# Performance work log

Measured on AMD Instinct MI355X. Metric: run time of the kernel, lower is better.

The kernel has to match this reference:

```python
import jax, jax.numpy as jnp
import numpy as np

N_IN = 512
N_OUT = 256
T = 2048
B = 32


def setup_inputs() -> dict:
    key = jax.random.key(0)
    ks = jax.random.split(key, 9)
    s_in = 1.0 / np.sqrt(N_IN)
    inp = {
        "xt": jax.random.normal(ks[0], (T, B, N_IN), dtype=jnp.float32),
        "ct_forward": jax.random.normal(ks[1], (1, B, N_OUT), dtype=jnp.float32),
        # weights stored torch-style as [out, in]
        "Wx": jax.random.uniform(ks[2], (N_OUT, N_IN), jnp.float32, -s_in, s_in),
        "Wf": jax.random.uniform(ks[3], (N_OUT, N_IN), jnp.float32, -s_in, s_in),
        "bf": jax.random.uniform(ks[4], (N_OUT,), jnp.float32, -s_in, s_in),
        "Wr": jax.random.uniform(ks[5], (N_OUT, N_IN), jnp.float32, -s_in, s_in),
        "br": jax.random.uniform(ks[6], (N_OUT,), jnp.float32, -s_in, s_in),
        "Wc": jax.random.uniform(ks[7], (N_OUT, N_IN), jnp.float32, -s_in, s_in),
        "bc": jax.random.uniform(ks[8], (N_OUT,), jnp.float32, -s_in, s_in),
    }
    return inp


def reference(xt, ct_forward, Wx, Wf, bf, Wr, br, Wc, bc):
    # Batched projections over all timesteps (the GEMM part of SRU).
    x_proj = jnp.einsum("tbi,oi->tbo", xt, Wx)              # [T,B,n_out]
    f = jax.nn.sigmoid(jnp.einsum("tbi,oi->tbo", xt, Wf) + bf)
    r = jax.nn.sigmoid(jnp.einsum("tbi,oi->tbo", xt, Wr) + br)
    cx = jnp.einsum("tbi,oi->tbo", xt, Wc) + bc

    def step(c, inp):
        x_t, ft, rt, cxt = inp
        c = ft * c + (1.0 - ft) * x_t
        h = rt * jnp.tanh(c) + (1.0 - rt) * cxt
        return c, h

    c_final, ht = jax.lax.scan(step, ct_forward[0], (x_proj, f, r, cx))
    # dropout=0.0 -> identity; forward returns (ht, ct)
    return ht, c_final
```

## Files before the change

### kernel.cpp

```cpp
#include <hip/hip_runtime.h>
#include <stdint.h>

#define T_STEPS 2048
#define BATCH   32
#define NIN     512
#define NOUT    256
#define MROWS   (T_STEPS*BATCH)
#define BO      (BATCH*NOUT)
#define NCHUNK  32
#define CHLEN   (T_STEPS/NCHUNK)

typedef _Float16 f16x8 __attribute__((ext_vector_type(8)));
typedef _Float16 f16x4 __attribute__((ext_vector_type(4)));
typedef float    fx4   __attribute__((ext_vector_type(4)));

#define LDSP(p) ((__attribute__((address_space(3))) void*)(p))
#define GLBP(p) ((const __attribute__((address_space(1))) void*)(p))

#define BAR()        asm volatile("s_barrier" ::: "memory")
#define WAITLGKM0()  do { asm volatile("s_waitcnt lgkmcnt(0)" ::: "memory"); __builtin_amdgcn_sched_barrier(0); } while(0)
#define WAITVM(n)    do { asm volatile("s_waitcnt vmcnt(" #n ")" ::: "memory"); __builtin_amdgcn_sched_barrier(0); } while(0)

__global__ __launch_bounds__(256) void convert_w(
    const float* __restrict__ Wx, const float* __restrict__ Wf,
    const float* __restrict__ Wr, const float* __restrict__ Wc,
    _Float16* __restrict__ Wcat)
{
    int idx = blockIdx.x * 256 + threadIdx.x;
    int n  = idx >> 7;
    int k4 = (idx & 127) * 4;
    int g = n >> 8, o = n & 255;
    const float* W = (g == 0) ? Wx : (g == 1) ? Wf : (g == 2) ? Wr : Wc;
    float4 v = *(const float4*)(W + o * NIN + k4);
    f16x4 h;
    h[0] = (_Float16)v.x; h[1] = (_Float16)v.y;
    h[2] = (_Float16)v.z; h[3] = (_Float16)v.w;
    *(f16x4*)(Wcat + n * NIN + k4) = h;
}

#define BM 256
#define BN 256
#define BK 64
#define NGT 32

__global__ __launch_bounds__(512, 1) void gemm_proj(
    const float*    __restrict__ xt,
    const _Float16* __restrict__ Wcat,
    const float* __restrict__ bfv, const float* __restrict__ brv, const float* __restrict__ bcv,
    _Float16* __restrict__ xp_h, _Float16* __restrict__ f_h,
    _Float16* __restrict__ r_h,  _Float16* __restrict__ cx_h)
{
    __shared__ char lds[131072];

    const int tid  = threadIdx.x;
    const int lane = tid & 63;
    const int w    = tid >> 6;
    const int wrq  = w >> 2;
    const int wcq  = w & 3;
    const int lr = lane & 15, lk = lane >> 4;

    int wg = (blockIdx.x & 7) * 32 + (blockIdx.x >> 3);
    const int  cg   = wg & 3;
    const int  mgrp = wg >> 2;
    const long m0 = (long)mgrp * 1024;
    const int  n0 = cg * BN;

    const char* baseAg = (const char*)xt + (m0 + (tid >> 4)) * 2048 + (tid & 15) * 16;
    const int awbase = (tid >> 4) * 128 + (((tid & 15) * 8) ^ (((tid >> 4) & 7) << 4));

    const int rl8  = lane >> 3;
    const int scol = (((lane & 7) ^ rl8) << 4);
    const char* baseB = (const char*)Wcat + ((long)(n0 + w * 8 + rl8)) * 1024 + scol;

    float4 av0[4], av1[4];
#define ALOAD_H(gi, half, dst) do {                                          \
        const char* _b = baseAg + (long)((gi) >> 3) * 524288                 \
                         + ((gi) & 7) * 256 + (half) * 262144;               \
        _Pragma("unroll")                                                    \
        for (int jj = 0; jj < 4; ++jj)                                       \
            dst[jj] = *(const float4*)(_b + jj * 65536);                     \
    } while (0)
#define AWRITE_H(gi, half, src) do {                                         \
        char* _d = lds + ((gi) & 1) * 32768 + (half) * 16384 + awbase;       \
        _Pragma("unroll")                                                    \
        for (int jj = 0; jj < 4; ++jj) {                                     \
            f16x4 _h;                                                        \
            _h[0] = (_Float16)src[jj].x; _h[1] = (_Float16)src[jj].y;        \
            _h[2] = (_Float16)src[jj].z; _h[3] = (_Float16)src[jj].w;        \
            *(f16x4*)(_d + jj * 4096) = _h;                                  \
        }                                                                    \
    } while (0)
#define STAGE_B(g, h) do {                                                   \
        char* _d = lds + 65536 + ((g) & 1) * 32768 + (h) * 16384 + w * 1024; \
        const char* _s = baseB + ((g) & 7) * 128 + (long)(h) * 131072;       \
        __builtin_amdgcn_global_load_lds(GLBP(_s),         LDSP(_d),        16, 0, 0); \
        __builtin_amdgcn_global_load_lds(GLBP(_s + 65536), LDSP(_d + 8192), 16, 0, 0); \
    } while (0)

    fx4 acc[2][2][4][2];
    #pragma unroll
    for (int a = 0; a < 2; ++a)
        #pragma unroll
        for (int b = 0; b < 2; ++b)
            #pragma unroll
            for (int c = 0; c < 4; ++c)
                #pragma unroll
                for (int d = 0; d < 2; ++d)
                    acc[a][b][c][d] = (fx4){0.f, 0.f, 0.f, 0.f};

    f16x8 Ar[4][2];
    f16x8 B0r[2][2];
    f16x8 B1r[2][2];

#define READ_A(c2, h) do {                                                   \
        _Pragma("unroll")                                                    \
        for (int mf = 0; mf < 4; ++mf) {                                     \
            int rl = wrq * 64 + mf * 16 + lr;                                \
            int rb = (c2) * 32768 + (h) * 16384 + rl * 128;                  \
            _Pragma("unroll")                                                \
            for (int kk = 0; kk < 2; ++kk)                                   \
                Ar[mf][kk] = *(const f16x8*)(lds + rb +                      \
                    ((kk * 64 + lk * 16) ^ ((rl & 7) << 4)));                \
        }                                                                    \
    } while (0)
#define READ_B(c2, h, dst) do {                                              \
        _Pragma("unroll")                                                    \
        for (int nf = 0; nf < 2; ++nf) {                                     \
            int rl = wcq * 32 + nf * 16 + lr;                                \
            int rb = 65536 + (c2) * 32768 + (h) * 16384 + rl * 128;          \
            _Pragma("unroll")                                                \
            for (int kk = 0; kk < 2; ++kk)                                   \
                dst[nf][kk] = *(const f16x8*)(lds + rb +                     \
                    ((kk * 64 + lk * 16) ^ ((rl & 7) << 4)));                \
        }                                                                    \
    } while (0)
#define MMACC(Qr, Qc, Br) do {                                               \
        __builtin_amdgcn_s_setprio(1);                                       \
        _Pragma("unroll")                                                    \
        for (int kk = 0; kk < 2; ++kk)                                       \
            _Pragma("unroll")                                                \
            for (int mf = 0; mf < 4; ++mf)                                   \
                _Pragma("unroll")                                            \
                for (int nf = 0; nf < 2; ++nf)                               \
                    acc[Qr][Qc][mf][nf] = __builtin_amdgcn_mfma_f32_16x16x32_f16( \
                        Br[nf][kk], Ar[mf][kk], acc[Qr][Qc][mf][nf], 0, 0, 0);    \
        __builtin_amdgcn_s_setprio(0);                                       \
    } while (0)

    const int g_out = cg;
    _Float16* outp = (g_out == 0) ? xp_h : (g_out == 1) ? f_h : (g_out == 2) ? r_h : cx_h;
    const float* bias = (g_out == 1) ? bfv : (g_out == 2) ? brv : (g_out == 3) ? bcv : nullptr;

    ALOAD_H(0, 0, av0); ALOAD_H(0, 1, av1);
    STAGE_B(0, 0); STAGE_B(0, 1);
    WAITVM(4);
    AWRITE_H(0, 0, av0); AWRITE_H(0, 1, av1);
    STAGE_B(1, 0);
    WAITVM(2);
    WAITLGKM0();
    BAR();

    for (int g = 0; g < NGT; ++g) {
        const int c2 = g & 1;
        READ_A(c2, 0);
        READ_B(c2, 0, B0r);
        if (g + 1 < NGT) { ALOAD_H(g + 1, 0, av0); STAGE_B(g + 1, 1); }
        WAITLGKM0();
        MMACC(0, 0, B0r);
        READ_B(c2, 1, B1r);
        if (g + 1 < NGT) ALOAD_H(g + 1, 1, av1);
        WAITLGKM0();
        MMACC(0, 1, B1r);
        READ_A(c2, 1);
        BAR();
        WAITLGKM0();
        MMACC(1, 0, B0r);
        if (g + 2 < NGT) STAGE_B(g + 2, 0);
        MMACC(1, 1, B1r);
        if (g + 2 < NGT) { WAITVM(2); } else { WAITVM(0); }
        if (g + 1 < NGT) { AWRITE_H(g + 1, 0, av0); AWRITE_H(g + 1, 1, av1); }
        WAITLGKM0();
        BAR();
        if ((g & 7) == 7) {
            const long mbase = m0 + (long)(g >> 3) * 256;
            #pragma unroll
            for (int Qr = 0; Qr < 2; ++Qr) {
                #pragma unroll
                for (int Qc = 0; Qc < 2; ++Qc) {
                    #pragma unroll
                    for (int nf = 0; nf < 2; ++nf) {
                        const int ob = Qc * 128 + wcq * 32 + nf * 16 + lk * 4;
                        float4 bv4 = (g_out == 0) ? (float4){0.f, 0.f, 0.f, 0.f}
                                                  : *(const float4*)(bias + ob);
                        #pragma unroll
                        for (int mf = 0; mf < 4; ++mf) {
                            long row = mbase + Qr * 128 + wrq * 64 + mf * 16 + lr;
                            fx4 v = acc[Qr][Qc][mf][nf];
                            f16x4 hv;
                            if (g_out == 1 || g_out == 2) {
                                float p0 = v[0] + bv4.x, p1 = v[1] + bv4.y;
                                float p2 = v[2] + bv4.z, p3 = v[3] + bv4.w;
                                hv[0] = (_Float16)(__builtin_amdgcn_rcpf(1.0f + __expf(-p0)));
                                hv[1] = (_Float16)(__builtin_amdgcn_rcpf(1.0f + __expf(-p1)));
                                hv[2] = (_Float16)(__builtin_amdgcn_rcpf(1.0f + __expf(-p2)));
                                hv[3] = (_Float16)(__builtin_amdgcn_rcpf(1.0f + __expf(-p3)));
                            } else {
                                hv[0] = (_Float16)(v[0] + bv4.x);
                                hv[1] = (_Float16)(v[1] + bv4.y);
                                hv[2] = (_Float16)(v[2] + bv4.z);
                                hv[3] = (_Float16)(v[3] + bv4.w);
                            }
                            *(f16x4*)(outp + row * NOUT + ob) = hv;
                            acc[Qr][Qc][mf][nf] = (fx4){0.f, 0.f, 0.f, 0.f};
                        }
                    }
                }
            }
        }
    }
}

__global__ __launch_bounds__(256) void chunk_scan_a(
    const _Float16* __restrict__ f_h, const _Float16* __restrict__ xp_h,
    float* __restrict__ chunkA, float* __restrict__ chunkB)
{
    int tid2 = blockIdx.x * 256 + threadIdx.x;
    int ch = tid2 >> 11;
    int b4 = (tid2 & 2047) << 2;
    long base = (long)ch * CHLEN * BO + b4;
    fx4 a = (fx4){1.f, 1.f, 1.f, 1.f};
    fx4 cc = (fx4){0.f, 0.f, 0.f, 0.f};
    for (int s = 0; s < CHLEN; ++s) {
        long i = base + (long)s * BO;
        f16x4 fv = *(const f16x4*)(f_h + i);
        f16x4 xv = *(const f16x4*)(xp_h + i);
        #pragma unroll
        for (int q = 0; q < 4; ++q) {
            float f = (float)fv[q], x = (float)xv[q];
            cc[q] = f * cc[q] + (1.f - f) * x;
            a[q] *= f;
        }
    }
    *(fx4*)(chunkA + ch * BO + b4) = a;
    *(fx4*)(chunkB + ch * BO + b4) = cc;
}

__global__ __launch_bounds__(256) void chunk_prop(
    const float* __restrict__ ct0,
    const float* __restrict__ chunkA, const float* __restrict__ chunkB,
    float* __restrict__ cin, float* __restrict__ c_final)
{
    int bo = blockIdx.x * 256 + threadIdx.x;
    float c = ct0[bo];
    #pragma unroll
    for (int ch = 0; ch < NCHUNK; ++ch) {
        cin[ch * BO + bo] = c;
        c = chunkA[ch * BO + bo] * c + chunkB[ch * BO + bo];
    }
    c_final[bo] = c;
}

__global__ __launch_bounds__(256) void chunk_scan_h(
    const _Float16* __restrict__ xp_h, const _Float16* __restrict__ f_h,
    const _Float16* __restrict__ r_h,  const _Float16* __restrict__ cx_h,
    const float* __restrict__ cin, float* __restrict__ ht)
{
    int tid2 = blockIdx.x * 256 + threadIdx.x;
    int ch = tid2 >> 11;
    int b4 = (tid2 & 2047) << 2;
    long base = (long)ch * CHLEN * BO + b4;
    fx4 c = *(const fx4*)(cin + ch * BO + b4);
    for (int s = 0; s < CHLEN; ++s) {
        long i = base + (long)s * BO;
        f16x4 fv  = *(const f16x4*)(f_h + i);
        f16x4 xv  = *(const f16x4*)(xp_h + i);
        f16x4 rv  = *(const f16x4*)(r_h + i);
        f16x4 cxv = *(const f16x4*)(cx_h + i);
        fx4 h4;
        #pragma unroll
        for (int q = 0; q < 4; ++q) {
            float f = (float)fv[q], x = (float)xv[q];
            float r = (float)rv[q], cx = (float)cxv[q];
            c[q] = f * c[q] + (1.f - f) * x;
            float e = __expf(2.f * c[q]);
            float th = (e - 1.f) * __builtin_amdgcn_rcpf(e + 1.f);
            h4[q] = r * th + (1.f - r) * cx;
        }
        *(fx4*)(ht + i) = h4;
    }
}

extern "C" void kernel_launch(void* const* d_in, const int* in_sizes, int n_in,
                              void* d_out, int out_size, void* d_ws, size_t ws_size,
                              hipStream_t stream) {
    const float* xt  = (const float*)d_in[0];
    const float* ct0 = (const float*)d_in[1];
    const float* Wx  = (const float*)d_in[2];
    const float* Wf  = (const float*)d_in[3];
    const float* bf_ = (const float*)d_in[4];
    const float* Wr  = (const float*)d_in[5];
    const float* br_ = (const float*)d_in[6];
    const float* Wc  = (const float*)d_in[7];
    const float* bc_ = (const float*)d_in[8];

    float* ht      = (float*)d_out;
    float* c_final = ht + (size_t)MROWS * NOUT;

    char* ws = (char*)d_ws;
    _Float16* Wcat = (_Float16*)ws;
    _Float16* xp_h = (_Float16*)(ws + (1 << 20));
    _Float16* f_h  = xp_h + (size_t)MROWS * NOUT;
    _Float16* r_h  = f_h  + (size_t)MROWS * NOUT;
    _Float16* cx_h = r_h  + (size_t)MROWS * NOUT;
    float* chunkA  = (float*)(cx_h + (size_t)MROWS * NOUT);
    float* chunkB  = chunkA + NCHUNK * BO;
    float* cin     = chunkB + NCHUNK * BO;

    convert_w<<<512, 256, 0, stream>>>(Wx, Wf, Wr, Wc, Wcat);
    gemm_proj<<<256, 512, 0, stream>>>(
        xt, Wcat, bf_, br_, bc_, xp_h, f_h, r_h, cx_h);
    chunk_scan_a<<<256, 256, 0, stream>>>(f_h, xp_h, chunkA, chunkB);
    chunk_prop<<<BO / 256, 256, 0, stream>>>(ct0, chunkA, chunkB, cin, c_final);
    chunk_scan_h<<<256, 256, 0, stream>>>(xp_h, f_h, r_h, cx_h, cin, ht);
}
```

Measured before the change: 183.8 us.

## Prefetch A tiles two stages ahead with double-buffered register sets

The GEMM main loop now issues global loads of the fp32 A tile two iterations ahead instead of one, alternating between two register buffers (sa/sb) by unrolling the loop by two. The vmcnt waits are loosened so the in-flight A loads overlap with a full tile of MFMA work, hiding global load latency. The cost is doubled register use for staging A, which may lower occupancy or cause spills.

Measured after the change: 335.7 us. 82.6% more time.

```diff
diff --git a/kernel.cpp b/kernel.cpp
--- a/kernel.cpp
+++ b/kernel.cpp
@@ -72,7 +72,8 @@
     const int scol = (((lane & 7) ^ rl8) << 4);
     const char* baseB = (const char*)Wcat + ((long)(n0 + w * 8 + rl8)) * 1024 + scol;
 
-    float4 av0[4], av1[4];
+    float4 sa_h0[4], sa_h1[4];
+    float4 sb_h0[4], sb_h1[4];
 #define ALOAD_H(gi, half, dst) do {                                          \
         const char* _b = baseAg + (long)((gi) >> 3) * 524288                 \
                          + ((gi) & 7) * 256 + (half) * 262144;               \
@@ -151,72 +152,83 @@
     _Float16* outp = (g_out == 0) ? xp_h : (g_out == 1) ? f_h : (g_out == 2) ? r_h : cx_h;
     const float* bias = (g_out == 1) ? bfv : (g_out == 2) ? brv : (g_out == 3) ? bcv : nullptr;
 
-    ALOAD_H(0, 0, av0); ALOAD_H(0, 1, av1);
+#define EPILOGUE(g) do {                                                     \
+        const long mbase = m0 + (long)((g) >> 3) * 256;                      \
+        _Pragma("unroll")                                                    \
+        for (int Qr = 0; Qr < 2; ++Qr)                                       \
+            _Pragma("unroll")                                                \
+            for (int Qc = 0; Qc < 2; ++Qc)                                   \
+                _Pragma("unroll")                                            \
+                for (int nf = 0; nf < 2; ++nf) {                             \
+                    const int ob = Qc * 128 + wcq * 32 + nf * 16 + lk * 4;   \
+                    float4 bv4 = (g_out == 0) ? (float4){0.f, 0.f, 0.f, 0.f} \
+                                              : *(const float4*)(bias + ob); \
+                    _Pragma("unroll")                                        \
+                    for (int mf = 0; mf < 4; ++mf) {                         \
+                        long row = mbase + Qr * 128 + wrq * 64 + mf * 16 + lr; \
+                        fx4 v = acc[Qr][Qc][mf][nf];                         \
+                        f16x4 hv;                                            \
+                        if (g_out == 1 || g_out == 2) {                      \
+                            float p0 = v[0] + bv4.x, p1 = v[1] + bv4.y;      \
+                            float p2 = v[2] + bv4.z, p3 = v[3] + bv4.w;      \
+                            hv[0] = (_Float16)(__builtin_amdgcn_rcpf(1.0f + __expf(-p0))); \
+                            hv[1] = (_Float16)(__builtin_amdgcn_rcpf(1.0f + __expf(-p1))); \
+                            hv[2] = (_Float16)(__builtin_amdgcn_rcpf(1.0f + __expf(-p2))); \
+                            hv[3] = (_Float16)(__builtin_amdgcn_rcpf(1.0f + __expf(-p3))); \
+                        } else {                                             \
+                            hv[0] = (_Float16)(v[0] + bv4.x);                \
+                            hv[1] = (_Float16)(v[1] + bv4.y);                \
+                            hv[2] = (_Float16)(v[2] + bv4.z);                \
+                            hv[3] = (_Float16)(v[3] + bv4.w);                \
+                        }                                                    \
+                        *(f16x4*)(outp + row * NOUT + ob) = hv;              \
+                        acc[Qr][Qc][mf][nf] = (fx4){0.f, 0.f, 0.f, 0.f};     \
+                    }                                                        \
+                }                                                            \
+    } while (0)
+
+#define TILE_BODY(g, WH0, WH1, LH0, LH1) do {                                \
+        const int c2 = (g) & 1;                                              \
+                                                                    \
+        READ_A(c2, 0);                                                       \
+        READ_B(c2, 0, B0r);                                                  \
+        if ((g) + 1 < NGT) STAGE_B((g) + 1, 1);                              \
+        if ((g) + 2 < NGT) ALOAD_H((g) + 2, 0, LH0);                         \
+        WAITLGKM0();                                                         \
+        MMACC(0, 0, B0r);                                                    \
+                                                                    \
+        READ_B(c2, 1, B1r);                                                  \
+        if ((g) + 2 < NGT) ALOAD_H((g) + 2, 1, LH1);                         \
+        WAITLGKM0();                                                         \
+        MMACC(0, 1, B1r);                                                    \
+                                                                    \
+        READ_A(c2, 1);                                                       \
+        BAR();                          \
+        WAITLGKM0();                                                         \
+        MMACC(1, 0, B0r);                                                    \
+                                                                    \
+        if ((g) + 2 < NGT) STAGE_B((g) + 2, 0);                              \
+        MMACC(1, 1, B1r);                                                    \
+        if ((g) + 2 < NGT) { WAITVM(10); } else { WAITVM(0); }               \
+        if ((g) + 1 < NGT) { AWRITE_H((g) + 1, 0, WH0); AWRITE_H((g) + 1, 1, WH1); } \
+        WAITLGKM0();                       \
+        BAR();                                            \
+        if (((g) & 7) == 7) EPILOGUE(g);                                     \
+    } while (0)
+
+    ALOAD_H(0, 0, sa_h0); ALOAD_H(0, 1, sa_h1);
     STAGE_B(0, 0); STAGE_B(0, 1);
     WAITVM(4);
-    AWRITE_H(0, 0, av0); AWRITE_H(0, 1, av1);
+    AWRITE_H(0, 0, sa_h0); AWRITE_H(0, 1, sa_h1);
+    ALOAD_H(1, 0, sb_h0); ALOAD_H(1, 1, sb_h1);
     STAGE_B(1, 0);
-    WAITVM(2);
+    WAITVM(10);
     WAITLGKM0();
     BAR();
 
-    for (int g = 0; g < NGT; ++g) {
-        const int c2 = g & 1;
-        READ_A(c2, 0);
-        READ_B(c2, 0, B0r);
-        if (g + 1 < NGT) { ALOAD_H(g + 1, 0, av0); STAGE_B(g + 1, 1); }
-        WAITLGKM0();
-        MMACC(0, 0, B0r);
-        READ_B(c2, 1, B1r);
-        if (g + 1 < NGT) ALOAD_H(g + 1, 1, av1);
-        WAITLGKM0();
-        MMACC(0, 1, B1r);
-        READ_A(c2, 1);
-        BAR();
-        WAITLGKM0();
-        MMACC(1, 0, B0r);
-        if (g + 2 < NGT) STAGE_B(g + 2, 0);
-        MMACC(1, 1, B1r);
-        if (g + 2 < NGT) { WAITVM(2); } else { WAITVM(0); }
-        if (g + 1 < NGT) { AWRITE_H(g + 1, 0, av0); AWRITE_H(g + 1, 1, av1); }
-        WAITLGKM0();
-        BAR();
-        if ((g & 7) == 7) {
-            const long mbase = m0 + (long)(g >> 3) * 256;
-            #pragma unroll
-            for (int Qr = 0; Qr < 2; ++Qr) {
-                #pragma unroll
-                for (int Qc = 0; Qc < 2; ++Qc) {
-                    #pragma unroll
-                    for (int nf = 0; nf < 2; ++nf) {
-                        const int ob = Qc * 128 + wcq * 32 + nf * 16 + lk * 4;
-                        float4 bv4 = (g_out == 0) ? (float4){0.f, 0.f, 0.f, 0.f}
-                                                  : *(const float4*)(bias + ob);
-                        #pragma unroll
-                        for (int mf = 0; mf < 4; ++mf) {
-                            long row = mbase + Qr * 128 + wrq * 64 + mf * 16 + lr;
-                            fx4 v = acc[Qr][Qc][mf][nf];
-                            f16x4 hv;
-                            if (g_out == 1 || g_out == 2) {
-                                float p0 = v[0] + bv4.x, p1 = v[1] + bv4.y;
-                                float p2 = v[2] + bv4.z, p3 = v[3] + bv4.w;
-                                hv[0] = (_Float16)(__builtin_amdgcn_rcpf(1.0f + __expf(-p0)));
-                                hv[1] = (_Float16)(__builtin_amdgcn_rcpf(1.0f + __expf(-p1)));
-                                hv[2] = (_Float16)(__builtin_amdgcn_rcpf(1.0f + __expf(-p2)));
-                                hv[3] = (_Float16)(__builtin_amdgcn_rcpf(1.0f + __expf(-p3)));
-                            } else {
-                                hv[0] = (_Float16)(v[0] + bv4.x);
-                                hv[1] = (_Float16)(v[1] + bv4.y);
-                                hv[2] = (_Float16)(v[2] + bv4.z);
-                                hv[3] = (_Float16)(v[3] + bv4.w);
-                            }
-                            *(f16x4*)(outp + row * NOUT + ob) = hv;
-                            acc[Qr][Qc][mf][nf] = (fx4){0.f, 0.f, 0.f, 0.f};
-                        }
-                    }
-                }
-            }
-        }
+    for (int gg = 0; gg < NGT; gg += 2) {
+        TILE_BODY(gg,     sb_h0, sb_h1, sa_h0, sa_h1);
+        TILE_BODY(gg + 1, sa_h0, sa_h1, sb_h0, sb_h1);
     }
 }
 
```
